# Optimization experiments

Hardware: AMD Instinct MI355X
Metric: run time of the kernel (lower is better)

## Reference

```python
import jax, jax.numpy as jnp
import numpy as np

HEADS = 8
TQ, QH, QW = 4, 16, 16
TK, KH, KW = 4, 16, 16
DIM = 64


def setup_inputs() -> dict:
    key = jax.random.key(0)
    k1, k2, k3, k4, k5 = jax.random.split(key, 5)
    return {
        "query": jax.random.normal(k1, (4, HEADS, TQ * QH * QW, DIM), dtype=jnp.float32),
        "scores": jax.random.normal(k2, (4, HEADS, TQ * QH * QW, TK * KH * KW), dtype=jnp.float32),
        "height_embeddings": jax.random.normal(k3, (2 * (max(QH, KH) - 1) + 1, DIM), dtype=jnp.float32),
        "width_embeddings": jax.random.normal(k4, (2 * (max(QW, KW) - 1) + 1, DIM), dtype=jnp.float32),
        "time_embeddings": jax.random.normal(k5, (2 * (max(TQ, TK) - 1) + 1, DIM), dtype=jnp.float32),
    }


def _rel_dist(q_n, k_n):
    # matches torch: ratios are both 1 when q_n == k_n
    q_ratio = round(max(k_n / q_n, 1.0))
    k_ratio = round(max(q_n / k_n, 1.0))
    d = jnp.arange(q_n)[:, None] * q_ratio - jnp.arange(k_n)[None, :] * k_ratio
    return d + (k_n - 1) * k_ratio  # [q_n, k_n] int indices


def reference(query, scores, height_embeddings, width_embeddings, time_embeddings):
    Rh = height_embeddings[_rel_dist(QH, KH)]  # [QH, KH, DIM]
    Rw = width_embeddings[_rel_dist(QW, KW)]   # [QW, KW, DIM]
    Rt = time_embeddings[_rel_dist(TQ, TK)]    # [TQ, TK, DIM]

    q = query.reshape(-1, HEADS, TQ, QH, QW, DIM)
    rel_h = jnp.einsum('bNthwc,hkc->bNthwk', q, Rh)  # [B,N,T,H,W,KH]
    rel_w = jnp.einsum('bNthwc,wkc->bNthwk', q, Rw)  # [B,N,T,H,W,KW]
    rel_t = jnp.einsum('bNthwc,tkc->bNthwk', q, Rt)  # [B,N,T,H,W,TK]

    s = scores.reshape(-1, HEADS, TQ, QH, QW, TK, KH, KW)
    s = (s
         + rel_h[:, :, :, :, :, None, :, None]
         + rel_w[:, :, :, :, :, None, None, :]
         + rel_t[:, :, :, :, :, :, None, None])
    return s.reshape(-1, HEADS, TQ * QH * QW, TK * KH * KW)
```

## Files before the change

### kernel.cpp

```cpp
#include <hip/hip_runtime.h>

#define NHEADS 8
#define TQ 4
#define QH 16
#define QW 16
#define TK 4
#define KH 16
#define KW 16
#define DIM 64
#define BATCH 4

typedef float f4 __attribute__((ext_vector_type(4)));

__global__ __launch_bounds__(256) void relpos_kernel(
    const float* __restrict__ query,
    const float* __restrict__ scores,
    const float* __restrict__ hemb,
    const float* __restrict__ wemb,
    const float* __restrict__ temb,
    float* __restrict__ out)
{
    const int tid  = threadIdx.x;
    const int row0 = blockIdx.x << 2;
    const int pos  = row0 & 1023;
    const int t  = pos >> 8;
    const int h  = (pos >> 4) & 15;
    const int w0 = pos & 15;

    const f4* sc4 = (const f4*)(scores + (size_t)row0 * 1024);
    f4 s0 = sc4[tid];
    f4 s1 = sc4[256 + tid];
    f4 s2 = sc4[512 + tid];
    f4 s3 = sc4[768 + tid];

    __shared__ float rel[4][36];

    if (tid < 144) {
        const int r = tid / 36;
        const int j = tid - r * 36;
        const float* emb;
        int e;
        if (j < 16)      { emb = hemb; e = h - j + 15; }
        else if (j < 32) { emb = wemb; e = (w0 + r) - (j - 16) + 15; }
        else             { emb = temb; e = t - (j - 32) + 3; }
        const float4* e4 = (const float4*)(emb + (size_t)e * DIM);
        const float4* q4 = (const float4*)(query + (size_t)(row0 + r) * DIM);
        float acc = 0.f;
#pragma unroll
        for (int c = 0; c < DIM / 4; ++c) {
            float4 qv = q4[c];
            float4 ev = e4[c];
            acc += qv.x * ev.x + qv.y * ev.y + qv.z * ev.z + qv.w * ev.w;
        }
        rel[r][j] = acc;
    }
    __syncthreads();

    const int base = tid << 2;
    const int tk  = base >> 8;
    const int kh  = (base >> 4) & 15;
    const int kw0 = base & 15;

    f4* o4 = (f4*)(out + (size_t)row0 * 1024);
#pragma unroll
    for (int r = 0; r < 4; ++r) {
        const f4 s = (r == 0) ? s0 : (r == 1) ? s1 : (r == 2) ? s2 : s3;
        const float a = rel[r][kh] + rel[r][32 + tk];
        f4 o;
        o.x = s.x + a + rel[r][16 + kw0 + 0];
        o.y = s.y + a + rel[r][16 + kw0 + 1];
        o.z = s.z + a + rel[r][16 + kw0 + 2];
        o.w = s.w + a + rel[r][16 + kw0 + 3];
        __builtin_nontemporal_store(o, o4 + r * 256 + tid);
    }
}

extern "C" void kernel_launch(void* const* d_in, const int* in_sizes, int n_in,
                              void* d_out, int out_size, void* d_ws, size_t ws_size,
                              hipStream_t stream) {
    const float* query  = (const float*)d_in[0];
    const float* scores = (const float*)d_in[1];
    const float* hemb   = (const float*)d_in[2];
    const float* wemb   = (const float*)d_in[3];
    const float* temb   = (const float*)d_in[4];
    float* out = (float*)d_out;

    const int rows = BATCH * NHEADS * TQ * QH * QW;
    relpos_kernel<<<dim3(rows / 4), dim3(256), 0, stream>>>(query, scores, hemb, wemb, temb, out);
}
```

Measured before the change: 252.8 us.

## Split bias computation into separate kernel and stream scores with precomputed biases

The single fused kernel is split in two. A bias kernel computes the relative-position dot products and writes per-row combined height+time biases (64 floats) and width biases (16 floats) to workspace. A streaming kernel then reads scores plus these small bias rows and writes the output with no dot-product work or block barrier. This takes the dot-product latency and __syncthreads off the bandwidth-bound path, at the cost of an extra launch and roughly 10MB of workspace write and read traffic. It falls back to the fused kernel if the workspace is too small.

```diff
diff --git a/kernel.cpp b/kernel.cpp
--- a/kernel.cpp
+++ b/kernel.cpp
@@ -10,7 +10,104 @@
 #define DIM 64
 #define BATCH 4
 
+#define ROWS (BATCH * NHEADS * TQ * QH * QW)
+#define WS_BYTES_NEEDED ((size_t)ROWS * 80 * sizeof(float))
+
 typedef float f4 __attribute__((ext_vector_type(4)));
+
+__global__ __launch_bounds__(256) void bias_kernel(
+    const float* __restrict__ query,
+    const float* __restrict__ hemb,
+    const float* __restrict__ wemb,
+    const float* __restrict__ temb,
+    float* __restrict__ ht,
+    f4* __restrict__ w4)
+{
+    const int tid  = threadIdx.x;
+    const int row0 = blockIdx.x << 2;
+    const int pos  = row0 & 1023;
+    const int t  = pos >> 8;
+    const int h  = (pos >> 4) & 15;
+    const int w0 = pos & 15;
+
+    __shared__ float rel[4][36];
+
+    if (tid < 144) {
+        const int r = tid / 36;
+        const int j = tid - r * 36;
+        const float* emb;
+        int e;
+        if (j < 16)      { emb = hemb; e = h - j + 15; }
+        else if (j < 32) { emb = wemb; e = (w0 + r) - (j - 16) + 15; }
+        else             { emb = temb; e = t - (j - 32) + 3; }
+        const float4* e4 = (const float4*)(emb + (size_t)e * DIM);
+        const float4* q4 = (const float4*)(query + (size_t)(row0 + r) * DIM);
+        float acc = 0.f;
+#pragma unroll
+        for (int c = 0; c < DIM / 4; ++c) {
+            float4 qv = q4[c];
+            float4 ev = e4[c];
+            acc += qv.x * ev.x + qv.y * ev.y + qv.z * ev.z + qv.w * ev.w;
+        }
+        rel[r][j] = acc;
+    }
+    __syncthreads();
+
+    {
+        const int r   = tid >> 6;
+        const int idx = tid & 63;
+        const int tk  = idx >> 4;
+        const int kh  = idx & 15;
+        ht[(size_t)(row0 + r) * 64 + idx] = rel[r][32 + tk] + rel[r][kh];
+    }
+    if (tid < 16) {
+        const int r = tid >> 2;
+        const int q = tid & 3;
+        f4 v;
+        v.x = rel[r][16 + 4 * q + 0];
+        v.y = rel[r][16 + 4 * q + 1];
+        v.z = rel[r][16 + 4 * q + 2];
+        v.w = rel[r][16 + 4 * q + 3];
+        w4[(size_t)(row0 + r) * 4 + q] = v;
+    }
+}
+
+__global__ __launch_bounds__(256) void stream_kernel(
+    const float* __restrict__ scores,
+    const float* __restrict__ ht,
+    const f4* __restrict__ w4,
+    float* __restrict__ out)
+{
+    const int tid  = threadIdx.x;
+    const int row0 = blockIdx.x << 2;
+
+    const f4* sc4 = (const f4*)(scores + (size_t)row0 * 1024);
+    f4 s0 = sc4[tid];
+    f4 s1 = sc4[256 + tid];
+    f4 s2 = sc4[512 + tid];
+    f4 s3 = sc4[768 + tid];
+
+    const int base = tid << 2;
+    const int hidx = ((base >> 8) << 4) | ((base >> 4) & 15);
+    const int wq   = tid & 3;
+
+    const float* htb = ht + (size_t)row0 * 64;
+    const f4*    wtb = w4 + (size_t)row0 * 4;
+    const float h0 = htb[hidx];
+    const float h1 = htb[64 + hidx];
+    const float h2 = htb[128 + hidx];
+    const float h3 = htb[192 + hidx];
+    const f4 v0 = wtb[wq];
+    const f4 v1 = wtb[4 + wq];
+    const f4 v2 = wtb[8 + wq];
+    const f4 v3 = wtb[12 + wq];
+
+    f4* o4 = (f4*)(out + (size_t)row0 * 1024);
+    __builtin_nontemporal_store(s0 + (v0 + h0), o4 + tid);
+    __builtin_nontemporal_store(s1 + (v1 + h1), o4 + 256 + tid);
+    __builtin_nontemporal_store(s2 + (v2 + h2), o4 + 512 + tid);
+    __builtin_nontemporal_store(s3 + (v3 + h3), o4 + 768 + tid);
+}
 
 __global__ __launch_bounds__(256) void relpos_kernel(
     const float* __restrict__ query,
@@ -85,6 +182,14 @@
     const float* temb   = (const float*)d_in[4];
     float* out = (float*)d_out;
 
-    const int rows = BATCH * NHEADS * TQ * QH * QW;
-    relpos_kernel<<<dim3(rows / 4), dim3(256), 0, stream>>>(query, scores, hemb, wemb, temb, out);
+    const int blocks = ROWS / 4;
+
+    if (d_ws != nullptr && ws_size >= WS_BYTES_NEEDED) {
+        float* ht = (float*)d_ws;
+        f4*    w4 = (f4*)((float*)d_ws + (size_t)ROWS * 64);
+        bias_kernel<<<dim3(blocks), dim3(256), 0, stream>>>(query, hemb, wemb, temb, ht, w4);
+        stream_kernel<<<dim3(blocks), dim3(256), 0, stream>>>(scores, ht, w4, out);
+    } else {
+        relpos_kernel<<<dim3(blocks), dim3(256), 0, stream>>>(query, scores, hemb, wemb, temb, out);
+    }
 }
```

New measurement: 287.1 us. 1.14x slower.
